# Optimization experiments

Measured on AMD Instinct MI355X. Metric: run time of the kernel, lower is better.

## Reference

```python
import jax, jax.numpy as jnp
import numpy as np

B, T, D, H = 4, 8192, 512, 512


def log_g(x):
    # log of the 'continuous relu-ish' gate: log(relu(x)+0.5) for x>=0, -softplus(-x) otherwise
    return jnp.where(x >= 0, jnp.log(jax.nn.relu(x) + 0.5), -jax.nn.softplus(-x))


def setup_inputs() -> dict:
    key = jax.random.key(0)
    ks = jax.random.split(key, 8)
    s = 1.0 / np.sqrt(D)
    return {
        "x": jax.random.normal(ks[0], (B, T, D), dtype=jnp.float32),
        "h_0": jax.random.normal(ks[1], (B, 1, H), dtype=jnp.float32),
        "W_f": jax.random.normal(ks[2], (D, H), dtype=jnp.float32) * s,
        "b_f": jnp.zeros((H,), dtype=jnp.float32),
        "W_i": jax.random.normal(ks[3], (D, H), dtype=jnp.float32) * s,
        "b_i": jnp.zeros((H,), dtype=jnp.float32),
        "W_h": jax.random.normal(ks[4], (D, H), dtype=jnp.float32) * s,
        "b_h": jnp.zeros((H,), dtype=jnp.float32),
    }


def reference(x, h_0, W_f, b_f, W_i, b_i, W_h, b_h):
    # three dense gate projections: [B,T,H]
    f_pre = jnp.einsum("btd,dh->bth", x, W_f) + b_f
    i_pre = jnp.einsum("btd,dh->bth", x, W_i) + b_i
    h_pre = jnp.einsum("btd,dh->bth", x, W_h) + b_h

    diff = jax.nn.softplus(-f_pre) - jax.nn.softplus(-i_pre)
    log_f = -jax.nn.softplus(diff)            # log forget gate  [B,T,H]
    log_i = -jax.nn.softplus(-diff)           # log input  gate  [B,T,H]

    log_h0 = log_g(h_0)                       # [B,1,H]
    log_tilde_h = log_g(h_pre)                # [B,T,H]
    log_values = jnp.concatenate([log_h0, log_i + log_tilde_h], axis=1)  # [B,T+1,H]

    # a_star[t] = sum_{s<=t} log_f[s], with a leading zero for the h_0 slot
    a_star = jnp.pad(jnp.cumsum(log_f, axis=1), ((0, 0), (1, 0), (0, 0)))  # [B,T+1,H]
    # stable parallel scan in log space
    log_h = a_star + jax.lax.cumlogsumexp(log_values - a_star, axis=1)     # [B,T+1,H]
    return jnp.exp(log_h)
```

## Files before the change

kernel.cpp:

```cpp
#include <hip/hip_runtime.h>
#include <hip/hip_bf16.h>

#define B_ 4
#define T_ 8192
#define D_ 512
#define H_ 512
#define M_ (B_ * T_)
#define CHUNK_ 128
#define NCHUNK_ (T_ / CHUNK_)
#define SEQS_ (B_ * H_)

typedef __attribute__((ext_vector_type(8))) short bf16x8;
typedef __attribute__((ext_vector_type(4))) float f32x4;

__device__ __forceinline__ unsigned short f2bf(float x) {
  union { float f; unsigned int u; } c; c.f = x;
  unsigned int u = c.u;
  unsigned int r = (u + 0x7fffu + ((u >> 16) & 1u)) >> 16;
  return (unsigned short)r;
}
__device__ __forceinline__ float bf2f(unsigned short h) {
  union { unsigned int u; float f; } c; c.u = ((unsigned int)h) << 16;
  return c.f;
}

__device__ __forceinline__ void gll16(const void* g, void* l) {
  __builtin_amdgcn_global_load_lds(
      (const __attribute__((address_space(1))) unsigned int*)g,
      (__attribute__((address_space(3))) unsigned int*)l, 16, 0, 0);
}

__global__ void wt_convert(const float* __restrict__ Wf, const float* __restrict__ Wi,
                           const float* __restrict__ Wh, unsigned short* __restrict__ Wt) {
  int e = blockIdx.x * 256 + threadIdx.x;
  int g = e >> 18;
  int rem = e & 262143;
  int k = rem >> 9;
  int n = rem & 511;
  const float* W = (g == 0) ? Wf : (g == 1) ? Wi : Wh;
  Wt[((size_t)g * H_ + n) * D_ + k] = f2bf(W[k * H_ + n]);
}

__global__ void x_convert(const float* __restrict__ x, unsigned short* __restrict__ xb) {
  size_t i = ((size_t)blockIdx.x * 256 + threadIdx.x) * 8;
  float4 a = *(const float4*)(x + i);
  float4 b = *(const float4*)(x + i + 4);
  ushort4 ha; ha.x = f2bf(a.x); ha.y = f2bf(a.y); ha.z = f2bf(a.z); ha.w = f2bf(a.w);
  ushort4 hb; hb.x = f2bf(b.x); hb.y = f2bf(b.y); hb.z = f2bf(b.z); hb.w = f2bf(b.w);
  *(ushort4*)(xb + i) = ha;
  *(ushort4*)(xb + i + 4) = hb;
}

__global__ __launch_bounds__(256, 2)
void gemm_gates(const unsigned short* __restrict__ xb, const unsigned short* __restrict__ Wt,
                const float* __restrict__ bF, const float* __restrict__ bI,
                const float* __restrict__ bH, unsigned int* __restrict__ AV) {
  __shared__ unsigned short xs[128 * 64];
  __shared__ unsigned short wsm[3 * 64 * 64];

  const int tid = threadIdx.x;
  const int hb = blockIdx.x;
  const int m0 = blockIdx.y * 128;
  const int n0 = hb * 64;
  const int wave = tid >> 6;
  const int lane = tid & 63;
  const int wm = (wave & 1) * 64;
  const int wn = (wave >> 1) * 32;
  const int l16 = lane & 15;
  const int quad = lane >> 4;

  const int lrow = lane >> 3;
  const int lch = (lane & 7) ^ lrow;

  int xoff[4];
  #pragma unroll
  for (int j = 0; j < 4; ++j) {
    const int gx = wave * 4 + j;
    xoff[j] = (m0 + gx * 8 + lrow) * D_ + lch * 8;
  }
  int woff[6], wdst[6];
  #pragma unroll
  for (int q = 0; q < 6; ++q) {
    const int gw = wave * 6 + q;
    const int g = gw >> 3, rg = gw & 7;
    woff[q] = (g * H_ + n0 + rg * 8 + lrow) * D_ + lch * 8;
    wdst[q] = g * 4096 + rg * 512;
  }

  f32x4 acc[3][4][2];
  #pragma unroll
  for (int g = 0; g < 3; ++g)
    #pragma unroll
    for (int mi = 0; mi < 4; ++mi)
      #pragma unroll
      for (int ni = 0; ni < 2; ++ni)
        acc[g][mi][ni] = (f32x4){0.f, 0.f, 0.f, 0.f};

  #pragma unroll 1
  for (int kb = 0; kb < D_; kb += 64) {
    #pragma unroll
    for (int j = 0; j < 4; ++j)
      gll16(xb + xoff[j] + kb, xs + (wave * 4 + j) * 512);
    #pragma unroll
    for (int q = 0; q < 6; ++q)
      gll16(Wt + woff[q] + kb, wsm + wdst[q]);
    __syncthreads();

    #pragma unroll
    for (int kk = 0; kk < 64; kk += 32) {
      const int kc = kk >> 3;
      bf16x8 af[4];
      #pragma unroll
      for (int mi = 0; mi < 4; ++mi) {
        const int r = wm + mi * 16 + l16;
        af[mi] = *(const bf16x8*)(xs + r * 64 + ((kc + quad) ^ (r & 7)) * 8);
      }
      bf16x8 bfr[3][2];
      #pragma unroll
      for (int g = 0; g < 3; ++g)
        #pragma unroll
        for (int ni = 0; ni < 2; ++ni) {
          const int r = wn + ni * 16 + l16;
          bfr[g][ni] = *(const bf16x8*)(wsm + g * 4096 + r * 64 + ((kc + quad) ^ (r & 7)) * 8);
        }
      #pragma unroll
      for (int g = 0; g < 3; ++g)
        #pragma unroll
        for (int mi = 0; mi < 4; ++mi)
          #pragma unroll
          for (int ni = 0; ni < 2; ++ni)
            acc[g][mi][ni] = __builtin_amdgcn_mfma_f32_16x16x32_bf16(
                af[mi], bfr[g][ni], acc[g][mi][ni], 0, 0, 0);
    }
    __syncthreads();
  }

  const size_t avbase = ((size_t)blockIdx.y * 8 + hb) * (CHUNK_ * 64);
  #pragma unroll
  for (int ni = 0; ni < 2; ++ni) {
    const int col = n0 + wn + ni * 16 + l16;
    const int hl = wn + ni * 16 + l16;
    const float bfv = bF[col], biv = bI[col], bhv = bH[col];
    #pragma unroll
    for (int mi = 0; mi < 4; ++mi) {
      const int tb = wm + mi * 16 + quad * 4;
      #pragma unroll
      for (int r = 0; r < 4; ++r) {
        float fp = acc[0][mi][ni][r] + bfv;
        float ip = acc[1][mi][ni][r] + biv;
        float hp = acc[2][mi][ni][r] + bhv;
        fp = fminf(fmaxf(fp, -30.f), 30.f);
        ip = fminf(fmaxf(ip, -30.f), 30.f);
        hp = fminf(fmaxf(hp, -30.f), 30.f);
        const float Ef = __expf(-fp);
        const float Ei = __expf(-ip);
        const float rr2 = 1.f / (2.f + Ef + Ei);
        const float fgate = (1.f + Ei) * rr2;
        const float igate = (1.f + Ef) * rr2;
        float gval;
        if (hp >= 0.f) gval = hp + 0.5f;
        else gval = 1.f / (1.f + __expf(-hp));
        const float vval = igate * gval;
        AV[avbase + (size_t)(tb + r) * 64 + hl] =
            (unsigned int)f2bf(fgate) | ((unsigned int)f2bf(vval) << 16);
      }
    }
  }
}

__global__ void scan_pass1(const unsigned int* __restrict__ AV,
                           float* __restrict__ Fc, float* __restrict__ Sc) {
  const int gid = blockIdx.x * 256 + threadIdx.x;
  const int hl = gid & 63;
  const int rest = gid >> 6;
  const int hbi = rest & 7;
  const int c = (rest >> 3) & 63;
  const int b = rest >> 9;
  const unsigned int* p = AV + (size_t)rest * (CHUNK_ * 64) + hl;
  float F = 1.f, S = 0.f;
  #pragma unroll 8
  for (int t = 0; t < CHUNK_; ++t) {
    unsigned int w = p[t * 64];
    float a = bf2f((unsigned short)(w & 0xffffu));
    float v = bf2f((unsigned short)(w >> 16));
    F *= a;
    S = fmaf(a, S, v);
  }
  const int s = b * 512 + hbi * 64 + hl;
  Fc[(size_t)s * NCHUNK_ + c] = F;
  Sc[(size_t)s * NCHUNK_ + c] = S;
}

__global__ void scan_pass2(const float* __restrict__ h0, const float* __restrict__ Fc,
                           const float* __restrict__ Sc, float* __restrict__ Hin,
                           float* __restrict__ out) {
  const int s = blockIdx.x * 256 + threadIdx.x;
  const int b = s >> 9;
  const int h = s & 511;
  float x = h0[s];
  float hcur = (x >= 0.f) ? (x + 0.5f) : (1.f / (1.f + __expf(-x)));
  out[(size_t)(b * (T_ + 1)) * H_ + h] = hcur;
  const float4* f4 = (const float4*)(Fc + (size_t)s * NCHUNK_);
  const float4* s4 = (const float4*)(Sc + (size_t)s * NCHUNK_);
  float4* hi4 = (float4*)(Hin + (size_t)s * NCHUNK_);
  #pragma unroll
  for (int cq = 0; cq < NCHUNK_ / 4; ++cq) {
    const float4 F = f4[cq];
    const float4 S = s4[cq];
    float4 Hv;
    Hv.x = hcur; hcur = fmaf(F.x, hcur, S.x);
    Hv.y = hcur; hcur = fmaf(F.y, hcur, S.y);
    Hv.z = hcur; hcur = fmaf(F.z, hcur, S.z);
    Hv.w = hcur; hcur = fmaf(F.w, hcur, S.w);
    hi4[cq] = Hv;
  }
}

__global__ void scan_pass3(const unsigned int* __restrict__ AV,
                           const float* __restrict__ Hin, float* __restrict__ out) {
  const int gid = blockIdx.x * 256 + threadIdx.x;
  const int hl = gid & 63;
  const int rest = gid >> 6;
  const int hbi = rest & 7;
  const int c = (rest >> 3) & 63;
  const int b = rest >> 9;
  const unsigned int* p = AV + (size_t)rest * (CHUNK_ * 64) + hl;
  float* o = out + ((size_t)(b * (T_ + 1) + c * CHUNK_ + 1) * H_) + hbi * 64 + hl;
  const int s = b * 512 + hbi * 64 + hl;
  float hcur = Hin[(size_t)s * NCHUNK_ + c];
  #pragma unroll 8
  for (int t = 0; t < CHUNK_; ++t) {
    unsigned int w = p[t * 64];
    float a = bf2f((unsigned short)(w & 0xffffu));
    float v = bf2f((unsigned short)(w >> 16));
    hcur = fmaf(a, hcur, v);
    o[(size_t)t * H_] = hcur;
  }
}

extern "C" void kernel_launch(void* const* d_in, const int* in_sizes, int n_in,
                              void* d_out, int out_size, void* d_ws, size_t ws_size,
                              hipStream_t stream) {
  const float* x  = (const float*)d_in[0];
  const float* h0 = (const float*)d_in[1];
  const float* Wf = (const float*)d_in[2];
  const float* bF = (const float*)d_in[3];
  const float* Wi = (const float*)d_in[4];
  const float* bI = (const float*)d_in[5];
  const float* Wh = (const float*)d_in[6];
  const float* bH = (const float*)d_in[7];
  float* out = (float*)d_out;

  char* ws = (char*)d_ws;
  size_t off = 0;
  unsigned int* AV = (unsigned int*)(ws + off);      off += (size_t)M_ * H_ * 4;
  unsigned short* xbf = (unsigned short*)(ws + off); off += (size_t)M_ * D_ * 2;
  unsigned short* Wt = (unsigned short*)(ws + off);  off += (size_t)3 * H_ * D_ * 2;
  float* Fc  = (float*)(ws + off); off += (size_t)NCHUNK_ * SEQS_ * 4;
  float* Sc  = (float*)(ws + off); off += (size_t)NCHUNK_ * SEQS_ * 4;
  float* Hin = (float*)(ws + off); off += (size_t)NCHUNK_ * SEQS_ * 4;

  wt_convert<<<(3 * H_ * D_) / 256, 256, 0, stream>>>(Wf, Wi, Wh, Wt);
  x_convert<<<(M_ * D_) / (256 * 8), 256, 0, stream>>>(x, xbf);
  gemm_gates<<<dim3(H_ / 64, M_ / 128), 256, 0, stream>>>(xbf, Wt, bF, bI, bH, AV);
  scan_pass1<<<(SEQS_ * NCHUNK_) / 256, 256, 0, stream>>>(AV, Fc, Sc);
  scan_pass2<<<SEQS_ / 256, 256, 0, stream>>>(h0, Fc, Sc, Hin, out);
  scan_pass3<<<(SEQS_ * NCHUNK_) / 256, 256, 0, stream>>>(AV, Hin, out);
}
```

Baseline: 248.3 us.

## Fuse chunk-scan reduction into GEMM epilogue and shrink scan chunks

The GEMM epilogue now stages packed gate/value pairs in a swizzled LDS tile and computes per-32-step chunk products and sums directly. This removes the separate scan_pass1 kernel and its full re-read of the AV buffer. Chunk summaries use a chunk-major layout so the sequential pass2 reads coalesce, and pass3 runs four times as many shorter segments for more parallelism. The weight transpose/convert kernel is vectorized to write four bf16 values per thread. The trade-offs are 32KB more LDS per GEMM block, which may affect occupancy, and a longer serial pass2 over 256 chunks.

Result: slower. 259.8 us (+4.6%).

```diff
diff --git a/kernel.cpp b/kernel.cpp
--- a/kernel.cpp
+++ b/kernel.cpp
@@ -7,7 +7,8 @@
 #define H_ 512
 #define M_ (B_ * T_)
 #define CHUNK_ 128
-#define NCHUNK_ (T_ / CHUNK_)
+#define SUB_ 32
+#define NSUB_ (T_ / SUB_)
 #define SEQS_ (B_ * H_)
 
 typedef __attribute__((ext_vector_type(8))) short bf16x8;
@@ -33,12 +34,17 @@
 __global__ void wt_convert(const float* __restrict__ Wf, const float* __restrict__ Wi,
                            const float* __restrict__ Wh, unsigned short* __restrict__ Wt) {
   int e = blockIdx.x * 256 + threadIdx.x;
-  int g = e >> 18;
-  int rem = e & 262143;
-  int k = rem >> 9;
-  int n = rem & 511;
+  int g = e >> 16;
+  int rem = e & 65535;
+  int n = rem >> 7;
+  int k4 = (rem & 127) * 4;
   const float* W = (g == 0) ? Wf : (g == 1) ? Wi : Wh;
-  Wt[((size_t)g * H_ + n) * D_ + k] = f2bf(W[k * H_ + n]);
+  ushort4 o;
+  o.x = f2bf(W[(k4 + 0) * H_ + n]);
+  o.y = f2bf(W[(k4 + 1) * H_ + n]);
+  o.z = f2bf(W[(k4 + 2) * H_ + n]);
+  o.w = f2bf(W[(k4 + 3) * H_ + n]);
+  *(ushort4*)(Wt + ((size_t)g * H_ + n) * D_ + k4) = o;
 }
 
 __global__ void x_convert(const float* __restrict__ x, unsigned short* __restrict__ xb) {
@@ -54,9 +60,11 @@
 __global__ __launch_bounds__(256, 2)
 void gemm_gates(const unsigned short* __restrict__ xb, const unsigned short* __restrict__ Wt,
                 const float* __restrict__ bF, const float* __restrict__ bI,
-                const float* __restrict__ bH, unsigned int* __restrict__ AV) {
+                const float* __restrict__ bH, unsigned int* __restrict__ AV,
+                float* __restrict__ Fc, float* __restrict__ Sc) {
   __shared__ unsigned short xs[128 * 64];
   __shared__ unsigned short wsm[3 * 64 * 64];
+  __shared__ unsigned int avs[128 * 64];
 
   const int tid = threadIdx.x;
   const int hb = blockIdx.x;
@@ -161,34 +169,33 @@
         if (hp >= 0.f) gval = hp + 0.5f;
         else gval = 1.f / (1.f + __expf(-hp));
         const float vval = igate * gval;
-        AV[avbase + (size_t)(tb + r) * 64 + hl] =
+        const int t = tb + r;
+        const unsigned int packed =
             (unsigned int)f2bf(fgate) | ((unsigned int)f2bf(vval) << 16);
+        AV[avbase + (size_t)t * 64 + hl] = packed;
+        avs[t * 64 + (hl ^ (((t >> 2) & 3) << 4))] = packed;
       }
     }
   }
-}
-
-__global__ void scan_pass1(const unsigned int* __restrict__ AV,
-                           float* __restrict__ Fc, float* __restrict__ Sc) {
-  const int gid = blockIdx.x * 256 + threadIdx.x;
-  const int hl = gid & 63;
-  const int rest = gid >> 6;
-  const int hbi = rest & 7;
-  const int c = (rest >> 3) & 63;
-  const int b = rest >> 9;
-  const unsigned int* p = AV + (size_t)rest * (CHUNK_ * 64) + hl;
+  __syncthreads();
+
+  const int seg = tid >> 6;
+  const int shl = tid & 63;
   float F = 1.f, S = 0.f;
   #pragma unroll 8
-  for (int t = 0; t < CHUNK_; ++t) {
-    unsigned int w = p[t * 64];
-    float a = bf2f((unsigned short)(w & 0xffffu));
-    float v = bf2f((unsigned short)(w >> 16));
+  for (int t = seg * SUB_; t < seg * SUB_ + SUB_; ++t) {
+    const unsigned int w = avs[t * 64 + (shl ^ (((t >> 2) & 3) << 4))];
+    const float a = bf2f((unsigned short)(w & 0xffffu));
+    const float v = bf2f((unsigned short)(w >> 16));
     F *= a;
     S = fmaf(a, S, v);
   }
-  const int s = b * 512 + hbi * 64 + hl;
-  Fc[(size_t)s * NCHUNK_ + c] = F;
-  Sc[(size_t)s * NCHUNK_ + c] = S;
+  const int bb = m0 >> 13;
+  const int cc = (m0 & 8191) >> 7;
+  const int sidx = cc * 4 + seg;
+  const int seq = bb * 512 + n0 + shl;
+  Fc[(size_t)sidx * SEQS_ + seq] = F;
+  Sc[(size_t)sidx * SEQS_ + seq] = S;
 }
 
 __global__ void scan_pass2(const float* __restrict__ h0, const float* __restrict__ Fc,
@@ -200,19 +207,10 @@
   float x = h0[s];
   float hcur = (x >= 0.f) ? (x + 0.5f) : (1.f / (1.f + __expf(-x)));
   out[(size_t)(b * (T_ + 1)) * H_ + h] = hcur;
-  const float4* f4 = (const float4*)(Fc + (size_t)s * NCHUNK_);
-  const float4* s4 = (const float4*)(Sc + (size_t)s * NCHUNK_);
-  float4* hi4 = (float4*)(Hin + (size_t)s * NCHUNK_);
-  #pragma unroll
-  for (int cq = 0; cq < NCHUNK_ / 4; ++cq) {
-    const float4 F = f4[cq];
-    const float4 S = s4[cq];
-    float4 Hv;
-    Hv.x = hcur; hcur = fmaf(F.x, hcur, S.x);
-    Hv.y = hcur; hcur = fmaf(F.y, hcur, S.y);
-    Hv.z = hcur; hcur = fmaf(F.z, hcur, S.z);
-    Hv.w = hcur; hcur = fmaf(F.w, hcur, S.w);
-    hi4[cq] = Hv;
+  #pragma unroll 8
+  for (int c = 0; c < NSUB_; ++c) {
+    Hin[(size_t)c * SEQS_ + s] = hcur;
+    hcur = fmaf(Fc[(size_t)c * SEQS_ + s], hcur, Sc[(size_t)c * SEQS_ + s]);
   }
 }
 
@@ -222,17 +220,20 @@
   const int hl = gid & 63;
   const int rest = gid >> 6;
   const int hbi = rest & 7;
-  const int c = (rest >> 3) & 63;
-  const int b = rest >> 9;
-  const unsigned int* p = AV + (size_t)rest * (CHUNK_ * 64) + hl;
-  float* o = out + ((size_t)(b * (T_ + 1) + c * CHUNK_ + 1) * H_) + hbi * 64 + hl;
-  const int s = b * 512 + hbi * 64 + hl;
-  float hcur = Hin[(size_t)s * NCHUNK_ + c];
+  const int sub = (rest >> 3) & 3;
+  const int c = (rest >> 5) & 63;
+  const int b = rest >> 11;
+  const unsigned int* p = AV + (size_t)((b * 64 + c) * 8 + hbi) * (CHUNK_ * 64)
+                             + sub * SUB_ * 64 + hl;
+  float* o = out + ((size_t)(b * (T_ + 1) + c * CHUNK_ + sub * SUB_ + 1) * H_)
+                 + hbi * 64 + hl;
+  const int seq = b * 512 + hbi * 64 + hl;
+  float hcur = Hin[(size_t)(c * 4 + sub) * SEQS_ + seq];
   #pragma unroll 8
-  for (int t = 0; t < CHUNK_; ++t) {
-    unsigned int w = p[t * 64];
-    float a = bf2f((unsigned short)(w & 0xffffu));
-    float v = bf2f((unsigned short)(w >> 16));
+  for (int t = 0; t < SUB_; ++t) {
+    const unsigned int w = p[t * 64];
+    const float a = bf2f((unsigned short)(w & 0xffffu));
+    const float v = bf2f((unsigned short)(w >> 16));
     hcur = fmaf(a, hcur, v);
     o[(size_t)t * H_] = hcur;
   }
@@ -256,14 +257,13 @@
   unsigned int* AV = (unsigned int*)(ws + off);      off += (size_t)M_ * H_ * 4;
   unsigned short* xbf = (unsigned short*)(ws + off); off += (size_t)M_ * D_ * 2;
   unsigned short* Wt = (unsigned short*)(ws + off);  off += (size_t)3 * H_ * D_ * 2;
-  float* Fc  = (float*)(ws + off); off += (size_t)NCHUNK_ * SEQS_ * 4;
-  float* Sc  = (float*)(ws + off); off += (size_t)NCHUNK_ * SEQS_ * 4;
-  float* Hin = (float*)(ws + off); off += (size_t)NCHUNK_ * SEQS_ * 4;
-
-  wt_convert<<<(3 * H_ * D_) / 256, 256, 0, stream>>>(Wf, Wi, Wh, Wt);
+  float* Fc  = (float*)(ws + off); off += (size_t)NSUB_ * SEQS_ * 4;
+  float* Sc  = (float*)(ws + off); off += (size_t)NSUB_ * SEQS_ * 4;
+  float* Hin = (float*)(ws + off); off += (size_t)NSUB_ * SEQS_ * 4;
+
+  wt_convert<<<(3 * H_ * D_ / 4) / 256, 256, 0, stream>>>(Wf, Wi, Wh, Wt);
   x_convert<<<(M_ * D_) / (256 * 8), 256, 0, stream>>>(x, xbf);
-  gemm_gates<<<dim3(H_ / 64, M_ / 128), 256, 0, stream>>>(xbf, Wt, bF, bI, bH, AV);
-  scan_pass1<<<(SEQS_ * NCHUNK_) / 256, 256, 0, stream>>>(AV, Fc, Sc);
+  gemm_gates<<<dim3(H_ / 64, M_ / 128), 256, 0, stream>>>(xbf, Wt, bF, bI, bH, AV, Fc, Sc);
   scan_pass2<<<SEQS_ / 256, 256, 0, stream>>>(h0, Fc, Sc, Hin, out);
-  scan_pass3<<<(SEQS_ * NCHUNK_) / 256, 256, 0, stream>>>(AV, Hin, out);
-}
+  scan_pass3<<<(SEQS_ * (T_ / SUB_)) / 256, 256, 0, stream>>>(AV, Hin, out);
+}
```
